# Kernel optimization log

Measured on AMD Instinct MI355X. Metric: run time of the kernel, lower is better.

The kernel has to match this reference:

```python
import jax, jax.numpy as jnp
import numpy as np

NBINS = 256


def _soft_weights(x):
    # Raised-cosine soft binning with unit bin width at integer centers 0..255.
    # Each value x contributes to bins floor(x) and floor(x)+1 with weights
    # w(d) = (1 + cos(pi*d)) / 2, which form a partition of unity.
    i0 = jnp.clip(jnp.floor(x), 0.0, NBINS - 1)
    d = x - i0
    w0 = 0.5 * (1.0 + jnp.cos(jnp.pi * d))
    i1 = jnp.clip(i0 + 1.0, 0.0, NBINS - 1)
    w1 = 1.0 - w0
    return i0.astype(jnp.int32), i1.astype(jnp.int32), w0, w1


def _cooccur_hist(a, b):
    # a, b: [N] float values of vertically-adjacent pixel pairs
    ia0, ia1, wa0, wa1 = _soft_weights(a)
    ib0, ib1, wb0, wb1 = _soft_weights(b)
    h = jnp.zeros((NBINS, NBINS), dtype=a.dtype)
    h = h.at[ia0, ib0].add(wa0 * wb0)
    h = h.at[ia0, ib1].add(wa0 * wb1)
    h = h.at[ia1, ib0].add(wa1 * wb0)
    h = h.at[ia1, ib1].add(wa1 * wb1)
    return h


def setup_inputs() -> dict:
    key = jax.random.key(0)
    B, C, H, W = 32, 3, 512, 512
    X = jax.random.uniform(key, (B, C, H, W), dtype=jnp.float32, minval=0.0, maxval=255.0)
    return {"X": X}


def reference(X):
    B, C, H, W = X.shape
    # img2pairs: pairs of vertically adjacent pixels per channel
    a = X[:, :, :-1, :].reshape(B * C, (H - 1) * W)
    b = X[:, :, 1:, :].reshape(B * C, (H - 1) * W)
    hists = jax.vmap(_cooccur_hist)(a, b).reshape(B, C, NBINS, NBINS)
    v_max = jnp.max(hists, axis=(2, 3))  # max over both histogram dims
    return hists / v_max[:, :, None, None]
```

## Files before the change

### kernel.cpp

```cpp
#include <hip/hip_runtime.h>

#define NBINS 256
constexpr int W_IMG = 512;
constexpr int H_IMG = 512;
constexpr int IMG_ELEMS = H_IMG * W_IMG;
constexpr int PAIR_ROWS = H_IMG - 1;
constexpr int NIMG = 96;
constexpr int HIST = NBINS * NBINS;
constexpr int GROUPS = 2;
constexpr int GROUP_ROWS = NBINS / GROUPS;
constexpr int LDSW = GROUP_ROWS * (NBINS / 2);
constexpr int WORDS_PER_IMG = HIST / 2;
constexpr int QI = 1024;
constexpr float QSCALE = 1024.0f;
constexpr float INVQ = 1.0f / 1024.0f;
constexpr int PF = 8;

__device__ __forceinline__ float cospi_fast(float d) {
    return __builtin_amdgcn_cosf(0.5f * d);
}

struct QElem {
    int i0;
    int q0, q1;
    int ga0, ga1;
    unsigned r0, r1;
};

__device__ __forceinline__ QElem quantize(float x, int lo) {
    QElem e;
    float fa = floorf(x);
    float w0 = 0.5f + 0.5f * cospi_fast(x - fa);
    e.i0 = (int)fa;
    e.q0 = (int)(w0 * QSCALE + 0.5f);
    e.q1 = QI - e.q0;
    int r0 = e.i0 - lo;
    e.ga0 = ((unsigned)r0 < (unsigned)GROUP_ROWS) ? e.q0 : 0;
    e.ga1 = ((unsigned)(r0 + 1) < (unsigned)GROUP_ROWS) ? e.q1 : 0;
    e.r0 = (unsigned)r0 & (GROUP_ROWS - 1);
    e.r1 = (unsigned)(r0 + 1) & (GROUP_ROWS - 1);
    return e;
}

__global__ __launch_bounds__(512, 4)
void hist_kernel(const float* __restrict__ X, unsigned* __restrict__ ws) {
    __shared__ unsigned lh[LDSW];
    const int tid = threadIdx.x;
    const int g = blockIdx.x;
    const int bc = blockIdx.y;
    const int s = blockIdx.z;
    const int S = gridDim.z;
    const int lo = g * GROUP_ROWS;
    const float* col = X + (size_t)bc * IMG_ELEMS + tid;

    {
        uint4* lv = reinterpret_cast<uint4*>(lh);
        for (int i = tid; i < LDSW / 4; i += 512) lv[i] = make_uint4(0u, 0u, 0u, 0u);
    }
    __syncthreads();

    const int r_beg = (PAIR_ROWS * s) / S;
    const int r_end = (PAIR_ROWS * (s + 1)) / S;

    float cur[PF], nxt[PF];
#pragma unroll
    for (int j = 0; j < PF; ++j)
        cur[j] = col[(size_t)min(r_beg + 1 + j, H_IMG - 1) * W_IMG];
    QElem a = quantize(col[(size_t)r_beg * W_IMG], lo);

    for (int R = r_beg; R < r_end; R += PF) {
#pragma unroll
        for (int j = 0; j < PF; ++j)
            nxt[j] = col[(size_t)min(R + PF + 1 + j, H_IMG - 1) * W_IMG];
#pragma unroll
        for (int j = 0; j < PF; ++j) {
            if (R + j < r_end) {
                QElem b = quantize(cur[j], lo);
                if (a.ga0 | a.ga1) {
                    unsigned p00 = (unsigned)(a.ga0 * b.q0 + QI / 2) >> 10;
                    unsigned p01 = (unsigned)(a.ga0 * b.q1 + QI / 2) >> 10;
                    unsigned p10 = (unsigned)(a.ga1 * b.q0 + QI / 2) >> 10;
                    unsigned p11 = (unsigned)(a.ga1 * b.q1 + QI / 2) >> 10;
                    unsigned c0 = (unsigned)b.i0 >> 1;
                    unsigned c1 = (unsigned)(b.i0 + 1) >> 1;
                    unsigned sh0 = ((unsigned)b.i0 & 1u) << 4;
                    unsigned sh1 = sh0 ^ 16u;
                    atomicAdd(&lh[a.r0 * (NBINS / 2) + c0], p00 << sh0);
                    atomicAdd(&lh[a.r0 * (NBINS / 2) + c1], p01 << sh1);
                    atomicAdd(&lh[a.r1 * (NBINS / 2) + c0], p10 << sh0);
                    atomicAdd(&lh[a.r1 * (NBINS / 2) + c1], p11 << sh1);
                }
                a = b;
            }
        }
#pragma unroll
        for (int j = 0; j < PF; ++j) cur[j] = nxt[j];
    }
    __syncthreads();

    unsigned* dst = ws + ((size_t)s * NIMG + bc) * WORDS_PER_IMG + (size_t)g * LDSW;
    const uint4* sv = reinterpret_cast<const uint4*>(lh);
    uint4* dv = reinterpret_cast<uint4*>(dst);
    for (int i = tid; i < LDSW / 4; i += 512) dv[i] = sv[i];
}

__global__ __launch_bounds__(256)
void merge_kernel(const unsigned* __restrict__ ws, float* __restrict__ out,
                  float* __restrict__ partial, int S) {
    const int bc = blockIdx.y;
    const int W0 = blockIdx.x * 1024;
    float2* o = reinterpret_cast<float2*>(out + (size_t)bc * HIST);
    float m = 0.0f;
    for (int i = threadIdx.x; i < 1024; i += 256) {
        const int W = W0 + i;
        unsigned sum = 0u;
        for (int s = 0; s < S; ++s)
            sum += ws[((size_t)s * NIMG + bc) * WORDS_PER_IMG + W];
        float v0 = (float)(sum & 0xFFFFu) * INVQ;
        float v1 = (float)(sum >> 16) * INVQ;
        o[W] = make_float2(v0, v1);
        m = fmaxf(m, fmaxf(v0, v1));
    }
#pragma unroll
    for (int off = 32; off > 0; off >>= 1) m = fmaxf(m, __shfl_down(m, off, 64));
    __shared__ float sm[4];
    if ((threadIdx.x & 63) == 0) sm[threadIdx.x >> 6] = m;
    __syncthreads();
    if (threadIdx.x == 0)
        partial[bc * 32 + blockIdx.x] = fmaxf(fmaxf(sm[0], sm[1]), fmaxf(sm[2], sm[3]));
}

__global__ void norm_kernel(float* __restrict__ out, const float* __restrict__ partial) {
    const int bc = blockIdx.y;
    float vm = 0.0f;
#pragma unroll
    for (int i = 0; i < 32; ++i) vm = fmaxf(vm, partial[bc * 32 + i]);
    const float inv = 1.0f / vm;
    float4* p = reinterpret_cast<float4*>(out + (size_t)bc * HIST);
    int i = blockIdx.x * blockDim.x + threadIdx.x;
    float4 v = p[i];
    v.x *= inv; v.y *= inv; v.z *= inv; v.w *= inv;
    p[i] = v;
}

extern "C" void kernel_launch(void* const* d_in, const int* in_sizes, int n_in,
                              void* d_out, int out_size, void* d_ws, size_t ws_size,
                              hipStream_t stream) {
    const float* X = (const float*)d_in[0];
    float* out = (float*)d_out;

    const size_t slice_bytes = (size_t)NIMG * WORDS_PER_IMG * sizeof(unsigned);
    int S = 4;
    while (S > 1 && ws_size < (size_t)S * slice_bytes + 16384) S >>= 1;

    unsigned* ws = (unsigned*)d_ws;
    float* partial = (float*)((char*)d_ws + (size_t)S * slice_bytes);

    hist_kernel<<<dim3(GROUPS, NIMG, S), 512, 0, stream>>>(X, ws);

    merge_kernel<<<dim3(32, NIMG), 256, 0, stream>>>(ws, out, partial, S);

    norm_kernel<<<dim3(64, NIMG), 256, 0, stream>>>(out, partial);
}
```

Before: 202.8 us.

## Use full-image LDS histogram per block and fuse merge with normalization

The histogram kernel now keeps the whole 256x256 packed histogram (128 KB) in dynamic LDS per 1024-thread block. Each pixel column is read once instead of once per row-group, and the per-group range checks go away. Rows are split into two halves across the block, and the row-slice count S rises to 8. The merge, max and normalize passes become a single kernel per image that sums the slices in registers, reduces the max and writes normalized output, which drops one full read-write pass over the output. The risk is lower occupancy, since LDS limits each CU to one such block, plus a large per-thread register array in the finale kernel; a fallback to the old two-group kernel is kept if the LDS attribute fails.

Measured after the change: 194.4 us. 4.2% less time.

```diff
diff --git a/kernel.cpp b/kernel.cpp
--- a/kernel.cpp
+++ b/kernel.cpp
@@ -7,27 +7,100 @@
 constexpr int PAIR_ROWS = H_IMG - 1;
 constexpr int NIMG = 96;
 constexpr int HIST = NBINS * NBINS;
-constexpr int GROUPS = 2;
-constexpr int GROUP_ROWS = NBINS / GROUPS;
-constexpr int LDSW = GROUP_ROWS * (NBINS / 2);
 constexpr int WORDS_PER_IMG = HIST / 2;
 constexpr int QI = 1024;
-constexpr float QSCALE = 1024.0f;
-constexpr float INVQ = 1.0f / 1024.0f;
 constexpr int PF = 8;
 
 __device__ __forceinline__ float cospi_fast(float d) {
     return __builtin_amdgcn_cosf(0.5f * d);
 }
 
+struct Q { int i0, q0; };
+
+__device__ __forceinline__ Q quant(float x) {
+    float fa = floorf(x);
+    Q e;
+    e.i0 = (int)fa;
+    e.q0 = (int)(cospi_fast(x - fa) * 512.0f + 512.5f);
+    return e;
+}
+
+__global__ __launch_bounds__(1024, 4)
+void hist1_kernel(const float* __restrict__ X, unsigned* __restrict__ ws) {
+    extern __shared__ unsigned lh[];
+    const int tid = threadIdx.x;
+    const int s = blockIdx.x;
+    const int bc = blockIdx.y;
+    const int S = gridDim.x;
+    const float* col = X + (size_t)bc * IMG_ELEMS + (tid & (W_IMG - 1));
+
+    {
+        uint4* lv = reinterpret_cast<uint4*>(lh);
+        for (int i = tid; i < WORDS_PER_IMG / 4; i += 1024)
+            lv[i] = make_uint4(0u, 0u, 0u, 0u);
+    }
+    __syncthreads();
+
+    const int rb = (PAIR_ROWS * s) / S;
+    const int re = (PAIR_ROWS * (s + 1)) / S;
+    const int l0 = (re - rb + 1) >> 1;
+    const int sub = tid >> 9;
+    const int r0t = rb + sub * l0;
+    const int r1t = sub ? re : rb + l0;
+
+    float cur[PF], nxt[PF];
+#pragma unroll
+    for (int j = 0; j < PF; ++j)
+        cur[j] = col[(size_t)min(r0t + 1 + j, PAIR_ROWS) * W_IMG];
+    Q a = quant(col[(size_t)r0t * W_IMG]);
+
+    for (int R = r0t; R < r1t; R += PF) {
+#pragma unroll
+        for (int j = 0; j < PF; ++j)
+            nxt[j] = col[(size_t)min(R + PF + 1 + j, PAIR_ROWS) * W_IMG];
+#pragma unroll
+        for (int j = 0; j < PF; ++j) {
+            if (R + j < r1t) {
+                Q b = quant(cur[j]);
+                int qa1 = QI - a.q0, qb1 = QI - b.q0;
+                unsigned p00 = (unsigned)(a.q0 * b.q0 + QI / 2) >> 10;
+                unsigned p01 = (unsigned)(a.q0 * qb1 + QI / 2) >> 10;
+                unsigned p10 = (unsigned)(qa1 * b.q0 + QI / 2) >> 10;
+                unsigned p11 = (unsigned)(qa1 * qb1 + QI / 2) >> 10;
+                unsigned c0 = (unsigned)b.i0 >> 1;
+                unsigned c1 = (unsigned)(b.i0 + 1) >> 1;
+                unsigned sh0 = ((unsigned)b.i0 & 1u) << 4;
+                unsigned sh1 = sh0 ^ 16u;
+                unsigned base0 = (unsigned)a.i0 << 7;
+                unsigned base1 = base0 + 128u;
+                atomicAdd(&lh[base0 + c0], p00 << sh0);
+                atomicAdd(&lh[base0 + c1], p01 << sh1);
+                atomicAdd(&lh[base1 + c0], p10 << sh0);
+                atomicAdd(&lh[base1 + c1], p11 << sh1);
+                a = b;
+            }
+        }
+#pragma unroll
+        for (int j = 0; j < PF; ++j) cur[j] = nxt[j];
+    }
+    __syncthreads();
+
+    unsigned* dst = ws + ((size_t)s * NIMG + bc) * WORDS_PER_IMG;
+    const uint4* sv = reinterpret_cast<const uint4*>(lh);
+    uint4* dv = reinterpret_cast<uint4*>(dst);
+    for (int i = tid; i < WORDS_PER_IMG / 4; i += 1024) dv[i] = sv[i];
+}
+
+constexpr int GROUP_ROWS = 128;
+constexpr int LDSW = GROUP_ROWS * (NBINS / 2);
+constexpr float QSCALE = 1024.0f;
+
 struct QElem {
-    int i0;
-    int q0, q1;
-    int ga0, ga1;
+    int i0, q0, q1, ga0, ga1;
     unsigned r0, r1;
 };
 
-__device__ __forceinline__ QElem quantize(float x, int lo) {
+__device__ __forceinline__ QElem quantize2(float x, int lo) {
     QElem e;
     float fa = floorf(x);
     float w0 = 0.5f + 0.5f * cospi_fast(x - fa);
@@ -43,7 +116,7 @@
 }
 
 __global__ __launch_bounds__(512, 4)
-void hist_kernel(const float* __restrict__ X, unsigned* __restrict__ ws) {
+void hist2_kernel(const float* __restrict__ X, unsigned* __restrict__ ws) {
     __shared__ unsigned lh[LDSW];
     const int tid = threadIdx.x;
     const int g = blockIdx.x;
@@ -65,17 +138,17 @@
     float cur[PF], nxt[PF];
 #pragma unroll
     for (int j = 0; j < PF; ++j)
-        cur[j] = col[(size_t)min(r_beg + 1 + j, H_IMG - 1) * W_IMG];
-    QElem a = quantize(col[(size_t)r_beg * W_IMG], lo);
+        cur[j] = col[(size_t)min(r_beg + 1 + j, PAIR_ROWS) * W_IMG];
+    QElem a = quantize2(col[(size_t)r_beg * W_IMG], lo);
 
     for (int R = r_beg; R < r_end; R += PF) {
 #pragma unroll
         for (int j = 0; j < PF; ++j)
-            nxt[j] = col[(size_t)min(R + PF + 1 + j, H_IMG - 1) * W_IMG];
+            nxt[j] = col[(size_t)min(R + PF + 1 + j, PAIR_ROWS) * W_IMG];
 #pragma unroll
         for (int j = 0; j < PF; ++j) {
             if (R + j < r_end) {
-                QElem b = quantize(cur[j], lo);
+                QElem b = quantize2(cur[j], lo);
                 if (a.ga0 | a.ga1) {
                     unsigned p00 = (unsigned)(a.ga0 * b.q0 + QI / 2) >> 10;
                     unsigned p01 = (unsigned)(a.ga0 * b.q1 + QI / 2) >> 10;
@@ -104,43 +177,49 @@
     for (int i = tid; i < LDSW / 4; i += 512) dv[i] = sv[i];
 }
 
-__global__ __launch_bounds__(256)
-void merge_kernel(const unsigned* __restrict__ ws, float* __restrict__ out,
-                  float* __restrict__ partial, int S) {
-    const int bc = blockIdx.y;
-    const int W0 = blockIdx.x * 1024;
+__global__ __launch_bounds__(1024, 4)
+void finale_kernel(const unsigned* __restrict__ ws, float* __restrict__ out, int S) {
+    const int bc = blockIdx.x;
+    const int tid = threadIdx.x;
+    const unsigned* base = ws + (size_t)bc * WORDS_PER_IMG;
+
+    unsigned sum[32];
+#pragma unroll
+    for (int k = 0; k < 32; ++k) sum[k] = 0u;
+    for (int s = 0; s < S; ++s) {
+        const unsigned* p = base + (size_t)s * NIMG * WORDS_PER_IMG;
+#pragma unroll
+        for (int k = 0; k < 32; ++k) sum[k] += p[tid + k * 1024];
+    }
+
+    float m = 0.0f;
+#pragma unroll
+    for (int k = 0; k < 32; ++k) {
+        m = fmaxf(m, (float)(sum[k] & 0xFFFFu));
+        m = fmaxf(m, (float)(sum[k] >> 16));
+    }
+#pragma unroll
+    for (int off = 32; off > 0; off >>= 1) m = fmaxf(m, __shfl_down(m, off, 64));
+    __shared__ float sm[16];
+    __shared__ float s_inv;
+    if ((tid & 63) == 0) sm[tid >> 6] = m;
+    __syncthreads();
+    if (tid == 0) {
+        float mm = sm[0];
+#pragma unroll
+        for (int i = 1; i < 16; ++i) mm = fmaxf(mm, sm[i]);
+        s_inv = 1.0f / mm;
+    }
+    __syncthreads();
+    const float inv = s_inv;
+
     float2* o = reinterpret_cast<float2*>(out + (size_t)bc * HIST);
-    float m = 0.0f;
-    for (int i = threadIdx.x; i < 1024; i += 256) {
-        const int W = W0 + i;
-        unsigned sum = 0u;
-        for (int s = 0; s < S; ++s)
-            sum += ws[((size_t)s * NIMG + bc) * WORDS_PER_IMG + W];
-        float v0 = (float)(sum & 0xFFFFu) * INVQ;
-        float v1 = (float)(sum >> 16) * INVQ;
-        o[W] = make_float2(v0, v1);
-        m = fmaxf(m, fmaxf(v0, v1));
-    }
-#pragma unroll
-    for (int off = 32; off > 0; off >>= 1) m = fmaxf(m, __shfl_down(m, off, 64));
-    __shared__ float sm[4];
-    if ((threadIdx.x & 63) == 0) sm[threadIdx.x >> 6] = m;
-    __syncthreads();
-    if (threadIdx.x == 0)
-        partial[bc * 32 + blockIdx.x] = fmaxf(fmaxf(sm[0], sm[1]), fmaxf(sm[2], sm[3]));
-}
-
-__global__ void norm_kernel(float* __restrict__ out, const float* __restrict__ partial) {
-    const int bc = blockIdx.y;
-    float vm = 0.0f;
-#pragma unroll
-    for (int i = 0; i < 32; ++i) vm = fmaxf(vm, partial[bc * 32 + i]);
-    const float inv = 1.0f / vm;
-    float4* p = reinterpret_cast<float4*>(out + (size_t)bc * HIST);
-    int i = blockIdx.x * blockDim.x + threadIdx.x;
-    float4 v = p[i];
-    v.x *= inv; v.y *= inv; v.z *= inv; v.w *= inv;
-    p[i] = v;
+#pragma unroll
+    for (int k = 0; k < 32; ++k) {
+        unsigned w = sum[k];
+        o[tid + k * 1024] = make_float2((float)(w & 0xFFFFu) * inv,
+                                        (float)(w >> 16) * inv);
+    }
 }
 
 extern "C" void kernel_launch(void* const* d_in, const int* in_sizes, int n_in,
@@ -148,17 +227,21 @@
                               hipStream_t stream) {
     const float* X = (const float*)d_in[0];
     float* out = (float*)d_out;
+    unsigned* ws = (unsigned*)d_ws;
 
     const size_t slice_bytes = (size_t)NIMG * WORDS_PER_IMG * sizeof(unsigned);
-    int S = 4;
-    while (S > 1 && ws_size < (size_t)S * slice_bytes + 16384) S >>= 1;
-
-    unsigned* ws = (unsigned*)d_ws;
-    float* partial = (float*)((char*)d_ws + (size_t)S * slice_bytes);
-
-    hist_kernel<<<dim3(GROUPS, NIMG, S), 512, 0, stream>>>(X, ws);
-
-    merge_kernel<<<dim3(32, NIMG), 256, 0, stream>>>(ws, out, partial, S);
-
-    norm_kernel<<<dim3(64, NIMG), 256, 0, stream>>>(out, partial);
-}
+    int S = 8;
+    while (S > 1 && (size_t)S * slice_bytes > ws_size) S >>= 1;
+
+    hipError_t attr_ok = hipFuncSetAttribute(
+        reinterpret_cast<const void*>(hist1_kernel),
+        hipFuncAttributeMaxDynamicSharedMemorySize, WORDS_PER_IMG * 4);
+
+    if (attr_ok == hipSuccess) {
+        hist1_kernel<<<dim3(S, NIMG), 1024, WORDS_PER_IMG * 4, stream>>>(X, ws);
+    } else {
+        hist2_kernel<<<dim3(2, NIMG, S), 512, 0, stream>>>(X, ws);
+    }
+
+    finale_kernel<<<NIMG, 1024, 0, stream>>>(ws, out, S);
+}
```
